# Kernel optimization log

Measured on AMD Instinct MI355X. Metric: run time of the kernel, lower is better.

The kernel has to match this reference:

```python
import jax, jax.numpy as jnp
import numpy as np
from jax import lax

B, T = 16, 1000
IN_DIM = 257
CTX = 3            # left + 1 + right
FEAT = CTX * IN_DIM  # 771
H = 512
L = 2              # SRU layers
KN = 9             # conv kernels
KS = 6             # conv kernel size


def setup_inputs() -> dict:
    key = jax.random.key(0)
    ks = jax.random.split(key, 10)
    n = jax.random.normal
    return {
        "inputs": n(ks[0], (B, T, FEAT), jnp.float32),
        "W_in": n(ks[1], (FEAT, H), jnp.float32) / np.sqrt(FEAT),
        "b_in": jnp.zeros((H,), jnp.float32),
        "W_rnn": n(ks[2], (L, H, 3 * H), jnp.float32) / np.sqrt(H),
        "v_rnn": n(ks[3], (L, 2 * H), jnp.float32) * 0.1,
        "b_rnn": jnp.zeros((L, 2 * H), jnp.float32),
        "conv_k": n(ks[4], (KN, 1, KS, KS), jnp.float32) * 0.05,
        "conv_b": jnp.zeros((KN,), jnp.float32),
        "W_out": n(ks[5], (H * KN, FEAT), jnp.float32) / np.sqrt(H * KN),
        "b_out": jnp.zeros((FEAT,), jnp.float32),
    }


def _sru_layer(x, W, v, b):
    # x: (T, B, H) time-major; SRU: c_t = f_t*c_{t-1} + (1-f_t)*(W x_t),
    # highway h_t = r_t*c_t + (1-r_t)*x_t; gates peek at c_{t-1} via v.
    U = jnp.einsum("tbh,hk->tbk", x, W)          # (T, B, 3H)
    xt, fp, rp = jnp.split(U, 3, axis=-1)
    vf, vr = jnp.split(v, 2)
    bf, br = jnp.split(b, 2)

    def step(c, inp):
        xt_t, fp_t, rp_t, xin_t = inp
        f = jax.nn.sigmoid(fp_t + vf * c + bf)
        c_new = f * c + (1.0 - f) * xt_t
        r = jax.nn.sigmoid(rp_t + vr * c + br)
        h = r * c_new + (1.0 - r) * xin_t
        return c_new, h

    c0 = jnp.zeros(x.shape[1:], x.dtype)
    _, hs = lax.scan(step, c0, (xt, fp, rp, x))
    return hs


def reference(inputs, W_in, b_in, W_rnn, v_rnn, b_rnn, conv_k, conv_b, W_out, b_out):
    # input layer: Linear + Tanh
    h = jnp.tanh(jnp.einsum("btf,fh->bth", inputs, W_in) + b_in)  # (B,T,H)
    x = jnp.transpose(h, (1, 0, 2))                               # (T,B,H)
    for l in range(L):
        x = _sru_layer(x, W_rnn[l], v_rnn[l], b_rnn[l])
    h = jnp.transpose(x, (1, 0, 2))[:, None]                      # (B,1,T,H)

    # Conv2d with asymmetric pad (left/top 3, right/bottom 2), +bias, tanh
    y = lax.conv_general_dilated(
        h, conv_k, window_strides=(1, 1), padding=[(3, 2), (3, 2)],
        dimension_numbers=("NCHW", "OIHW", "NCHW"))
    y = jnp.tanh(y + conv_b[None, :, None, None])                 # (B,KN,T,H)
    # MaxPool2d(3, stride=1, padding=1)
    y = lax.reduce_window(y, -jnp.inf, lax.max, (1, 1, 3, 3), (1, 1, 1, 1),
                          [(0, 0), (0, 0), (1, 1), (1, 1)])

    # (B,KN,T,H) -> (B,T,H,KN) -> (B,T,H*KN)  (matches torch double transpose)
    y = jnp.transpose(y, (0, 2, 3, 1)).reshape(B, T, H * KN)
    mask = jax.nn.sigmoid(jnp.einsum("btf,fo->bto", y, W_out) + b_out)
    out = mask * inputs
    return out[:, :, IN_DIM:2 * IN_DIM]  # center frame (left_context slice)
```

## Files before the change

### kernel.cpp

```cpp
#include <hip/hip_runtime.h>
#include <hip/hip_bf16.h>

#define B_    16
#define T_    1000
#define FEAT  771
#define FEATP 800
#define H_    512
#define H3    1536
#define KN_   9
#define KHID  4608
#define M_    16000
#define NOUT  257
#define KSLICES 3

typedef _Float16 half8 __attribute__((ext_vector_type(8)));
typedef _Float16 half4 __attribute__((ext_vector_type(4)));
typedef _Float16 half2v __attribute__((ext_vector_type(2)));
typedef _Float16 h2 __attribute__((ext_vector_type(2)));
typedef float    floatx4 __attribute__((ext_vector_type(4)));

__device__ inline float tanh_fast(float z) {
    return 1.0f - 2.0f / (1.0f + __expf(2.0f * z));
}
__device__ inline float sigmoid_fast(float z) {
    return 1.0f / (1.0f + __expf(-z));
}

__device__ inline void gload16(const _Float16* g, _Float16* l) {
    __builtin_amdgcn_global_load_lds(
        (const __attribute__((address_space(1))) void*)g,
        (__attribute__((address_space(3))) void*)l, 16, 0, 0);
}

__device__ inline void pk_fma_acc(unsigned& acc, unsigned w, unsigned x) {
    asm("v_pk_fma_f16 %0, %1, %2, %0" : "+v"(acc) : "s"(w), "v"(x));
}
__device__ inline unsigned pk_max(unsigned a, unsigned b) {
    unsigned d;
    asm("v_pk_max_f16 %0, %1, %2" : "=v"(d) : "v"(a), "v"(b));
    return d;
}

__global__ void convert_inputs(const float* __restrict__ in, _Float16* __restrict__ A1) {
    size_t i = (size_t)blockIdx.x * 256 + threadIdx.x;
    if (i >= (size_t)M_ * FEATP) return;
    size_t r = i / FEATP;
    int   cc = (int)(i % FEATP);
    A1[i] = (cc < FEAT) ? (_Float16)in[r * FEAT + cc] : (_Float16)0.f;
}

__global__ void pack_ck(const float* __restrict__ ck, unsigned int* __restrict__ ckp) {
    const int i = threadIdx.x;
    if (i < 9 * 36) {
        const _Float16 w = (_Float16)ck[i];
        const unsigned short u = __builtin_bit_cast(unsigned short, w);
        ckp[i] = ((unsigned int)u << 16) | u;
    }
}

__global__ __launch_bounds__(256) void transpose_w(
    const float* __restrict__ W, _Float16* __restrict__ Wt,
    int K, int N, int ldw, int coloff, int Kp, int perm9)
{
    __shared__ float tile[32][33];
    const int kb = blockIdx.x * 32;
    const int nb = blockIdx.y * 32;
    const int tx = threadIdx.x & 31;
    const int ty = threadIdx.x >> 5;
    #pragma unroll
    for (int r = ty; r < 32; r += 8) {
        const int k = kb + r, n = nb + tx;
        tile[r][tx] = (k < K && n < N) ? W[(size_t)k * ldw + coloff + n] : 0.f;
    }
    __syncthreads();
    #pragma unroll
    for (int r = ty; r < 32; r += 8) {
        const int n = nb + r, k = kb + tx;
        if (n < N && k < Kp) {
            size_t kidx = (size_t)k;
            if (perm9) kidx = (size_t)(k % 9) * 512 + (size_t)(k / 9);
            Wt[(size_t)n * Kp + kidx] = (_Float16)tile[tx][r];
        }
    }
}

template <int EPI>
__global__ __launch_bounds__(256) void gemm_kernel(
    const _Float16* __restrict__ A, const _Float16* __restrict__ Bt,
    int Kp, int nk, int Nb,
    _Float16* __restrict__ Ch, float* __restrict__ Cf, int ldc,
    const float* __restrict__ bias)
{
    __shared__ __align__(16) _Float16 As[2][128][32];
    __shared__ __align__(16) _Float16 Bs[2][128][32];

    const int tid  = threadIdx.x;
    const int m0   = blockIdx.x * 128;
    const int n0   = blockIdx.y * 128;
    const int koff = blockIdx.z * (nk << 5);
    const int wave = tid >> 6;
    const int lane = tid & 63;
    const int wr   = (wave >> 1) << 6;
    const int wc   = (wave & 1) << 6;
    const int lrow = lane & 15;
    const int lq   = lane >> 4;

    const int srow0  = wave * 32 + (lane >> 2);
    const int schunk = (lane & 3) * 8;
    const _Float16* aSrc = A  + (size_t)(m0 + srow0) * Kp + koff + schunk;
    const _Float16* bSrc = Bt + (size_t)(n0 + srow0) * Kp + koff + schunk;
    const size_t rstep = (size_t)16 * Kp;

    floatx4 acc[4][4];
    #pragma unroll
    for (int i = 0; i < 4; ++i)
        #pragma unroll
        for (int j = 0; j < 4; ++j)
            #pragma unroll
            for (int r = 0; r < 4; ++r) acc[i][j][r] = 0.f;

    gload16(aSrc,         &As[0][wave * 32][0]);
    gload16(aSrc + rstep, &As[0][wave * 32 + 16][0]);
    gload16(bSrc,         &Bs[0][wave * 32][0]);
    gload16(bSrc + rstep, &Bs[0][wave * 32 + 16][0]);
    asm volatile("s_waitcnt vmcnt(0)" ::: "memory");
    __builtin_amdgcn_s_barrier();

    for (int kc = 0; kc < nk; ++kc) {
        const int cur = kc & 1;
        if (kc + 1 < nk) {
            const _Float16* a2 = aSrc + (size_t)(kc + 1) * 32;
            const _Float16* b2 = bSrc + (size_t)(kc + 1) * 32;
            gload16(a2,         &As[cur ^ 1][wave * 32][0]);
            gload16(a2 + rstep, &As[cur ^ 1][wave * 32 + 16][0]);
            gload16(b2,         &Bs[cur ^ 1][wave * 32][0]);
            gload16(b2 + rstep, &Bs[cur ^ 1][wave * 32 + 16][0]);
        }

        half8 af[4], bfr[4];
        #pragma unroll
        for (int i = 0; i < 4; ++i) af[i]  = *(const half8*)(&As[cur][wr + i * 16 + lrow][lq * 8]);
        #pragma unroll
        for (int j = 0; j < 4; ++j) bfr[j] = *(const half8*)(&Bs[cur][wc + j * 16 + lrow][lq * 8]);
        #pragma unroll
        for (int i = 0; i < 4; ++i)
            #pragma unroll
            for (int j = 0; j < 4; ++j)
                acc[i][j] = __builtin_amdgcn_mfma_f32_16x16x32_f16(af[i], bfr[j], acc[i][j], 0, 0, 0);

        if (kc + 1 < nk) {
            asm volatile("s_waitcnt vmcnt(0)" ::: "memory");
            __builtin_amdgcn_s_barrier();
        }
    }

    #pragma unroll
    for (int j = 0; j < 4; ++j) {
        const int col = n0 + wc + j * 16 + lrow;
        if (col >= Nb) continue;
        #pragma unroll
        for (int i = 0; i < 4; ++i) {
            #pragma unroll
            for (int r = 0; r < 4; ++r) {
                const int row = m0 + wr + i * 16 + lq * 4 + r;
                float v = acc[i][j][r];
                if constexpr (EPI == 0) {
                    float z = v + bias[col];
                    Ch[(size_t)row * ldc + col] = (_Float16)tanh_fast(z);
                } else if constexpr (EPI == 1) {
                    Ch[(size_t)(col >> 9) * ((size_t)M_ * 512) + (size_t)row * 512 + (col & 511)] = (_Float16)v;
                } else {
                    Cf[(size_t)blockIdx.z * M_ * NOUT + (size_t)row * NOUT + col] = v;
                }
            }
        }
    }
}

__global__ __launch_bounds__(256) void reduce_out(
    const float* __restrict__ Cp, const float* __restrict__ bias,
    const float* __restrict__ aux, float* __restrict__ out)
{
    const size_t i = (size_t)blockIdx.x * 256 + threadIdx.x;
    if (i >= (size_t)M_ * NOUT) return;
    const int row = (int)(i / NOUT);
    const int col = (int)(i % NOUT);
    float s = Cp[i] + Cp[i + (size_t)M_ * NOUT] + Cp[i + 2 * (size_t)M_ * NOUT];
    out[i] = sigmoid_fast(s + bias[col]) * aux[(size_t)row * FEAT + 257 + col];
}

__global__ __launch_bounds__(256) void repack_u(
    const _Float16* __restrict__ U,
    const _Float16* __restrict__ X,
    _Float16* __restrict__ Upk)
{
    const size_t i = (size_t)blockIdx.x * 256 + threadIdx.x;
    if (i >= (size_t)M_ * 128) return;
    const size_t base = i << 2;
    const half4 a = *(const half4*)(U + base);
    const half4 f = *(const half4*)(U + (size_t)M_ * 512 + base);
    const half4 r = *(const half4*)(U + 2 * (size_t)M_ * 512 + base);
    const half4 x = *(const half4*)(X + base);
    half8 lo, hi;
    lo[0] = a[0]; lo[1] = f[0]; lo[2] = r[0]; lo[3] = x[0];
    lo[4] = a[1]; lo[5] = f[1]; lo[6] = r[1]; lo[7] = x[1];
    hi[0] = a[2]; hi[1] = f[2]; hi[2] = r[2]; hi[3] = x[2];
    hi[4] = a[3]; hi[5] = f[3]; hi[6] = r[3]; hi[7] = x[3];
    *(half8*)(Upk + base * 4)     = lo;
    *(half8*)(Upk + base * 4 + 8) = hi;
}

__global__ __launch_bounds__(64) void sru_scan(
    const _Float16* __restrict__ Upk, _Float16* __restrict__ Xout,
    const float* __restrict__ v, const float* __restrict__ bg)
{
    const int gid = blockIdx.x * 64 + threadIdx.x;
    const int b = gid >> 9;
    const int h = gid & 511;
    const float vf = v[h],      vr = v[512 + h];
    const float bf = bg[h],     br = bg[512 + h];

    const _Float16* p = Upk + ((size_t)b * T_ * 512 + h) * 4;
    _Float16* ox = Xout + (size_t)b * T_ * 512 + h;

    half4 buf[20];
    #pragma unroll
    for (int j = 0; j < 20; ++j) buf[j] = *(const half4*)(p + (size_t)j * 2048);

    float c = 0.f;
    for (int t0 = 0; t0 < T_; t0 += 20) {
        #pragma unroll
        for (int j = 0; j < 20; ++j) {
            const int t = t0 + j;
            const half4 cur = buf[j];
            const int tn = t + 20;
            if (tn < T_) buf[j] = *(const half4*)(p + (size_t)tn * 2048);
            const float xt = (float)cur[0];
            const float fp = (float)cur[1];
            const float rp = (float)cur[2];
            const float x  = (float)cur[3];
            const float f  = sigmoid_fast(fp + vf * c + bf);
            const float r  = sigmoid_fast(rp + vr * c + br);
            const float cn = f * c + (1.0f - f) * xt;
            const float hO = r * cn + (1.0f - r) * x;
            ox[(size_t)t * 512] = (_Float16)hO;
            c = cn;
        }
    }
}

#define CVW 76

__global__ __launch_bounds__(320) void conv_pool(
    const _Float16* __restrict__ X, const unsigned int* __restrict__ ckp,
    const float* __restrict__ cb, _Float16* __restrict__ A3)
{
    __shared__ __align__(16) _Float16 in_s[23][80];
    __shared__ __align__(16) _Float16 cv[9][18][CVW];
    const int tid = threadIdx.x;
    int bi = blockIdx.x;
    const int th = bi & 7;  bi >>= 3;
    const int tt = bi % 63;
    const int b  = bi / 63;
    const int t0 = tt * 16, h0 = th * 64;

    for (int i = tid; i < 23 * 76; i += 320) {
        const int r = i / 76, cc = i % 76;
        const int gt = t0 - 4 + r, gh = h0 - 4 + cc;
        _Float16 val = (_Float16)0.f;
        if (gt >= 0 && gt < T_ && gh >= 0 && gh < H_)
            val = X[((size_t)b * T_ + gt) * H_ + gh];
        in_s[r][cc] = val;
    }
    __syncthreads();

    if (tid < 306) {
        const int pt = tid / 17;
        const int co = (tid % 17) * 4;

        const int ct = t0 - 1 + pt;
        const bool rok = (ct >= 0) && (ct < T_);
        const int chb = h0 - 1 + co;
        const bool ok0 = rok && (chb + 0 >= 0) && (chb + 0 < H_);
        const bool ok1 = rok && (chb + 1 >= 0) && (chb + 1 < H_);
        const bool ok2 = rok && (chb + 2 >= 0) && (chb + 2 < H_);
        const bool ok3 = rok && (chb + 3 >= 0) && (chb + 3 < H_);

        unsigned acc0[9], acc1[9];
        #pragma unroll
        for (int k = 0; k < 9; ++k) { acc0[k] = 0u; acc1[k] = 0u; }

        #pragma unroll 1
        for (int ii = 0; ii < 6; ++ii) {
            const unsigned int* rw = (const unsigned int*)&in_s[pt + ii][co];
            const uint2 a01 = *(const uint2*)(rw);
            const uint2 a23 = *(const uint2*)(rw + 2);
            const unsigned int A0 = a01.x, A1v = a01.y, A2 = a23.x, A3v = a23.y;
            const unsigned int A4 = rw[4];
            const unsigned int M0 = __builtin_amdgcn_alignbit(A1v, A0, 16);
            const unsigned int M1 = __builtin_amdgcn_alignbit(A2, A1v, 16);
            const unsigned int M2 = __builtin_amdgcn_alignbit(A3v, A2, 16);
            const unsigned int M3 = __builtin_amdgcn_alignbit(A4, A3v, 16);

            const unsigned int* wt = ckp + ii * 6;
            #pragma unroll
            for (int k = 0; k < 9; ++k) {
                const unsigned int* wk = wt + k * 36;
                pk_fma_acc(acc0[k], wk[0], A0);   pk_fma_acc(acc1[k], wk[0], A1v);
                pk_fma_acc(acc0[k], wk[1], M0);   pk_fma_acc(acc1[k], wk[1], M1);
                pk_fma_acc(acc0[k], wk[2], A1v);  pk_fma_acc(acc1[k], wk[2], A2);
                pk_fma_acc(acc0[k], wk[3], M1);   pk_fma_acc(acc1[k], wk[3], M2);
                pk_fma_acc(acc0[k], wk[4], A2);   pk_fma_acc(acc1[k], wk[4], A3v);
                pk_fma_acc(acc0[k], wk[5], M2);   pk_fma_acc(acc1[k], wk[5], M3);
            }
        }

        const _Float16 NEG = (_Float16)(-65504.f);
        #pragma unroll
        for (int k = 0; k < 9; ++k) {
            const h2 pa = __builtin_bit_cast(h2, acc0[k]);
            const h2 pb = __builtin_bit_cast(h2, acc1[k]);
            half4 o;
            o[0] = ok0 ? pa[0] : NEG;
            o[1] = ok1 ? pa[1] : NEG;
            o[2] = ok2 ? pb[0] : NEG;
            o[3] = ok3 ? pb[1] : NEG;
            *(half4*)(&cv[k][pt][co]) = o;
        }
    }
    __syncthreads();

    if (tid < 256) {
        const int pt = tid >> 4;
        const int gt = t0 + pt;
        if (gt < T_) {
            const int ph = (tid & 15) * 4;
            _Float16* dst = A3 + ((size_t)b * T_ + gt) * KHID + (h0 + ph);
            #pragma unroll
            for (int k = 0; k < 9; ++k) {
                unsigned q01 = 0xFC00FC00u, q23 = 0xFC00FC00u;
                #pragma unroll
                for (int dr = 0; dr < 3; ++dr) {
                    const unsigned* cr = (const unsigned*)&cv[k][pt + dr][ph];
                    const uint2 w01 = *(const uint2*)(cr);
                    const unsigned w2 = cr[2];
                    const unsigned m12 = __builtin_amdgcn_alignbit(w01.y, w01.x, 16);
                    const unsigned m34 = __builtin_amdgcn_alignbit(w2, w01.y, 16);
                    q01 = pk_max(q01, pk_max(pk_max(w01.x, m12), w01.y));
                    q23 = pk_max(q23, pk_max(pk_max(w01.y, m34), w2));
                }
                const h2 qa = __builtin_bit_cast(h2, q01);
                const h2 qb = __builtin_bit_cast(h2, q23);
                const float bk = cb[k];
                half4 o;
                o[0] = (_Float16)tanh_fast((float)qa[0] + bk);
                o[1] = (_Float16)tanh_fast((float)qa[1] + bk);
                o[2] = (_Float16)tanh_fast((float)qb[0] + bk);
                o[3] = (_Float16)tanh_fast((float)qb[1] + bk);
                *(half4*)(dst + (size_t)k * 512) = o;
            }
        }
    }
}

extern "C" void kernel_launch(void* const* d_in, const int* in_sizes, int n_in,
                              void* d_out, int out_size, void* d_ws, size_t ws_size,
                              hipStream_t stream) {
    const float* inputs = (const float*)d_in[0];
    const float* W_in   = (const float*)d_in[1];
    const float* b_in   = (const float*)d_in[2];
    const float* W_rnn  = (const float*)d_in[3];
    const float* v_rnn  = (const float*)d_in[4];
    const float* b_rnn  = (const float*)d_in[5];
    const float* conv_k = (const float*)d_in[6];
    const float* conv_b = (const float*)d_in[7];
    const float* W_out  = (const float*)d_in[8];
    const float* b_out  = (const float*)d_in[9];
    float* out = (float*)d_out;

    char* ws = (char*)d_ws;
    size_t off = 0;
    auto take = [&](size_t bytes) -> char* {
        off = (off + 255) & ~(size_t)255;
        char* p = ws + off;
        off += bytes;
        return p;
    };
    _Float16* W3T  = (_Float16*)take((size_t)NOUT * KHID * 2);
    _Float16* A1   = (_Float16*)take((size_t)M_ * FEATP * 2);
    _Float16* W1T  = (_Float16*)take((size_t)H_ * FEATP * 2);
    _Float16* W2T0 = (_Float16*)take((size_t)H3 * H_ * 2);
    _Float16* W2T1 = (_Float16*)take((size_t)H3 * H_ * 2);
    _Float16* X0   = (_Float16*)take((size_t)M_ * H_ * 2);
    _Float16* X1   = (_Float16*)take((size_t)M_ * H_ * 2);
    _Float16* U    = (_Float16*)take(3 * (size_t)M_ * 512 * 2);
    _Float16* A3   = (_Float16*)take((size_t)M_ * KHID * 2);
    unsigned int* ckp = (unsigned int*)take(9 * 36 * 4);
    _Float16* Upk = A3;
    float* Cp = (float*)A1;
    _Float16* X2 = X0;

    {
        size_t n = (size_t)M_ * FEATP;
        convert_inputs<<<dim3((unsigned)((n + 255) / 256)), 256, 0, stream>>>(inputs, A1);
    }
    pack_ck<<<dim3(1), 384, 0, stream>>>(conv_k, ckp);
    transpose_w<<<dim3(25, 16), 256, 0, stream>>>(W_in, W1T, FEAT, H_, H_, 0, FEATP, 0);
    transpose_w<<<dim3(16, 48), 256, 0, stream>>>(W_rnn, W2T0, H_, H3, H3, 0, H_, 0);
    transpose_w<<<dim3(16, 48), 256, 0, stream>>>(W_rnn + (size_t)H_ * H3, W2T1, H_, H3, H3, 0, H_, 0);
    transpose_w<<<dim3(144, 9), 256, 0, stream>>>(W_out, W3T, KHID, NOUT, FEAT, 257, KHID, 1);

    const unsigned nrep = (unsigned)(((size_t)M_ * 128 + 255) / 256);

    gemm_kernel<0><<<dim3(125, 4), 256, 0, stream>>>(A1, W1T, FEATP, 25, H_, X0, nullptr, H_, b_in);

    gemm_kernel<1><<<dim3(125, 12), 256, 0, stream>>>(X0, W2T0, H_, 16, H3, U, nullptr, 0, nullptr);
    repack_u<<<dim3(nrep), 256, 0, stream>>>(U, X0, Upk);
    sru_scan<<<dim3(128), 64, 0, stream>>>(Upk, X1, v_rnn, b_rnn);

    gemm_kernel<1><<<dim3(125, 12), 256, 0, stream>>>(X1, W2T1, H_, 16, H3, U, nullptr, 0, nullptr);
    repack_u<<<dim3(nrep), 256, 0, stream>>>(U, X1, Upk);
    sru_scan<<<dim3(128), 64, 0, stream>>>(Upk, X2, v_rnn + 1024, b_rnn + 1024);

    conv_pool<<<dim3(16 * 63 * 8), 320, 0, stream>>>(X2, ckp, conv_b, A3);

    gemm_kernel<3><<<dim3(125, 3, KSLICES), 256, 0, stream>>>(A3, W3T, KHID, 144 / KSLICES, NOUT, nullptr, Cp, 0, nullptr);
    {
        const unsigned nred = (unsigned)(((size_t)M_ * NOUT + 255) / 256);
        reduce_out<<<dim3(nred), 256, 0, stream>>>(Cp, b_out + 257, inputs, out);
    }
}
```

Measured before the change: 803.1 us.

## Drop repack kernel; stage SRU gate planes through double-buffered LDS in scan

After: 727.0 us. -9.5%, faster.

```diff
diff --git a/kernel.cpp b/kernel.cpp
--- a/kernel.cpp
+++ b/kernel.cpp
@@ -189,63 +189,68 @@
     out[i] = sigmoid_fast(s + bias[col]) * aux[(size_t)row * FEAT + 257 + col];
 }
 
-__global__ __launch_bounds__(256) void repack_u(
+__global__ __launch_bounds__(64) void sru_scan(
     const _Float16* __restrict__ U,
     const _Float16* __restrict__ X,
-    _Float16* __restrict__ Upk)
-{
-    const size_t i = (size_t)blockIdx.x * 256 + threadIdx.x;
-    if (i >= (size_t)M_ * 128) return;
-    const size_t base = i << 2;
-    const half4 a = *(const half4*)(U + base);
-    const half4 f = *(const half4*)(U + (size_t)M_ * 512 + base);
-    const half4 r = *(const half4*)(U + 2 * (size_t)M_ * 512 + base);
-    const half4 x = *(const half4*)(X + base);
-    half8 lo, hi;
-    lo[0] = a[0]; lo[1] = f[0]; lo[2] = r[0]; lo[3] = x[0];
-    lo[4] = a[1]; lo[5] = f[1]; lo[6] = r[1]; lo[7] = x[1];
-    hi[0] = a[2]; hi[1] = f[2]; hi[2] = r[2]; hi[3] = x[2];
-    hi[4] = a[3]; hi[5] = f[3]; hi[6] = r[3]; hi[7] = x[3];
-    *(half8*)(Upk + base * 4)     = lo;
-    *(half8*)(Upk + base * 4 + 8) = hi;
-}
-
-__global__ __launch_bounds__(64) void sru_scan(
-    const _Float16* __restrict__ Upk, _Float16* __restrict__ Xout,
+    _Float16* __restrict__ Xout,
     const float* __restrict__ v, const float* __restrict__ bg)
 {
-    const int gid = blockIdx.x * 64 + threadIdx.x;
-    const int b = gid >> 9;
-    const int h = gid & 511;
-    const float vf = v[h],      vr = v[512 + h];
-    const float bf = bg[h],     br = bg[512 + h];
-
-    const _Float16* p = Upk + ((size_t)b * T_ * 512 + h) * 4;
+    __shared__ __align__(16) _Float16 lds[2][4][40][64];
+    const int tid = threadIdx.x;
+    const int b   = blockIdx.x >> 3;
+    const int h0  = (blockIdx.x & 7) << 6;
+    const int h   = h0 + tid;
+    const float vf = v[h],       vr = v[512 + h];
+    const float bf = bg[h],      br = bg[512 + h];
+
+    const _Float16* plane0 = U;
+    const _Float16* plane1 = U + (size_t)M_ * 512;
+    const _Float16* plane2 = U + 2 * (size_t)M_ * 512;
+    const _Float16* plane3 = X;
+
+    const int lrow = tid >> 3;
+    const int lcol = (tid & 7) * 8;
+
     _Float16* ox = Xout + (size_t)b * T_ * 512 + h;
 
-    half4 buf[20];
-    #pragma unroll
-    for (int j = 0; j < 20; ++j) buf[j] = *(const half4*)(p + (size_t)j * 2048);
-
+    auto refill = [&](int bufi, int t0) {
+        const size_t rbase = (size_t)(b * T_ + t0 + lrow) * 512 + h0 + lcol;
+        #pragma unroll
+        for (int j = 0; j < 5; ++j) {
+            const size_t o = rbase + (size_t)(8 * j) * 512;
+            gload16(plane0 + o, &lds[bufi][0][8 * j][0]);
+            gload16(plane1 + o, &lds[bufi][1][8 * j][0]);
+            gload16(plane2 + o, &lds[bufi][2][8 * j][0]);
+            gload16(plane3 + o, &lds[bufi][3][8 * j][0]);
+        }
+    };
+
+    refill(0, 0);
     float c = 0.f;
-    for (int t0 = 0; t0 < T_; t0 += 20) {
-        #pragma unroll
-        for (int j = 0; j < 20; ++j) {
-            const int t = t0 + j;
-            const half4 cur = buf[j];
-            const int tn = t + 20;
-            if (tn < T_) buf[j] = *(const half4*)(p + (size_t)tn * 2048);
-            const float xt = (float)cur[0];
-            const float fp = (float)cur[1];
-            const float rp = (float)cur[2];
-            const float x  = (float)cur[3];
+    int cur = 0;
+    for (int tb = 0; tb < 25; ++tb) {
+        const int t0 = tb * 40;
+        if (tb + 1 < 25) {
+            refill(cur ^ 1, t0 + 40);
+            asm volatile("s_waitcnt vmcnt(20)" ::: "memory");
+        } else {
+            asm volatile("s_waitcnt vmcnt(0)" ::: "memory");
+        }
+        __builtin_amdgcn_sched_barrier(0);
+        #pragma unroll
+        for (int j = 0; j < 40; ++j) {
+            const float xt = (float)lds[cur][0][j][tid];
+            const float fp = (float)lds[cur][1][j][tid];
+            const float rp = (float)lds[cur][2][j][tid];
+            const float x  = (float)lds[cur][3][j][tid];
             const float f  = sigmoid_fast(fp + vf * c + bf);
             const float r  = sigmoid_fast(rp + vr * c + br);
             const float cn = f * c + (1.0f - f) * xt;
             const float hO = r * cn + (1.0f - r) * x;
-            ox[(size_t)t * 512] = (_Float16)hO;
+            ox[(size_t)(t0 + j) * 512] = (_Float16)hO;
             c = cn;
         }
+        cur ^= 1;
     }
 }
 
@@ -396,7 +401,6 @@
     _Float16* U    = (_Float16*)take(3 * (size_t)M_ * 512 * 2);
     _Float16* A3   = (_Float16*)take((size_t)M_ * KHID * 2);
     unsigned int* ckp = (unsigned int*)take(9 * 36 * 4);
-    _Float16* Upk = A3;
     float* Cp = (float*)A1;
     _Float16* X2 = X0;
 
@@ -410,17 +414,13 @@
     transpose_w<<<dim3(16, 48), 256, 0, stream>>>(W_rnn + (size_t)H_ * H3, W2T1, H_, H3, H3, 0, H_, 0);
     transpose_w<<<dim3(144, 9), 256, 0, stream>>>(W_out, W3T, KHID, NOUT, FEAT, 257, KHID, 1);
 
-    const unsigned nrep = (unsigned)(((size_t)M_ * 128 + 255) / 256);
-
     gemm_kernel<0><<<dim3(125, 4), 256, 0, stream>>>(A1, W1T, FEATP, 25, H_, X0, nullptr, H_, b_in);
 
     gemm_kernel<1><<<dim3(125, 12), 256, 0, stream>>>(X0, W2T0, H_, 16, H3, U, nullptr, 0, nullptr);
-    repack_u<<<dim3(nrep), 256, 0, stream>>>(U, X0, Upk);
-    sru_scan<<<dim3(128), 64, 0, stream>>>(Upk, X1, v_rnn, b_rnn);
+    sru_scan<<<dim3(128), 64, 0, stream>>>(U, X0, X1, v_rnn, b_rnn);
 
     gemm_kernel<1><<<dim3(125, 12), 256, 0, stream>>>(X1, W2T1, H_, 16, H3, U, nullptr, 0, nullptr);
-    repack_u<<<dim3(nrep), 256, 0, stream>>>(U, X1, Upk);
-    sru_scan<<<dim3(128), 64, 0, stream>>>(Upk, X2, v_rnn + 1024, b_rnn + 1024);
+    sru_scan<<<dim3(128), 64, 0, stream>>>(U, X1, X2, v_rnn + 1024, b_rnn + 1024);
 
     conv_pool<<<dim3(16 * 63 * 8), 320, 0, stream>>>(X2, ckp, conv_b, A3);
 
```
